# Performance work log

Hardware: AMD Instinct MI355X
Metric: run time of the kernel (lower is better)

The kernel has to match this reference:

```python
import jax, jax.numpy as jnp
import numpy as np

N = 100000
E = 1600000
H = 128
M = 256
L = 6
G = 512          # number of graphs in the batch
A = 95           # num_atom_types
EXTRA = 3        # input_dim - 1
EPS = 1e-5


def swish(x):
    return x * jax.nn.sigmoid(x)


def setup_inputs() -> dict:
    key = jax.random.key(0)
    ks = jax.random.split(key, 16)
    z = jax.random.randint(ks[0], (N, 1), 0, A).astype(jnp.float32)
    extra = jax.random.normal(ks[1], (N, EXTRA), dtype=jnp.float32)
    x = jnp.concatenate([z, extra], axis=1)                     # [N, 4]
    edge_index = jax.random.randint(ks[2], (2, E), 0, N)        # [2, E]
    batch = jnp.sort(jax.random.randint(ks[3], (N,), 0, G))     # [N]
    s = 0.02
    z_embed = jax.random.normal(ks[4], (A, H), dtype=jnp.float32) * s
    extra_w = jax.random.normal(ks[5], (H, EXTRA), dtype=jnp.float32) * (1.0 / np.sqrt(EXTRA))
    extra_b = jnp.zeros((H,), jnp.float32)
    conv_w = jax.random.normal(ks[6], (L, H, H), dtype=jnp.float32) * (1.0 / np.sqrt(H))
    conv_b = jnp.zeros((L, H), jnp.float32)
    gamma = jnp.ones((L, H), jnp.float32)
    beta = jnp.zeros((L, H), jnp.float32)
    mean_scale = jnp.ones((L, H), jnp.float32)
    mlp_w1 = jax.random.normal(ks[7], (L, M, H), dtype=jnp.float32) * (1.0 / np.sqrt(H))
    mlp_b1 = jnp.zeros((L, M), jnp.float32)
    mlp_w2 = jax.random.normal(ks[8], (L, H, M), dtype=jnp.float32) * (1.0 / np.sqrt(M))
    mlp_b2 = jnp.zeros((L, H), jnp.float32)
    return dict(x=x, edge_index=edge_index, batch=batch, z_embed=z_embed,
                extra_w=extra_w, extra_b=extra_b, conv_w=conv_w, conv_b=conv_b,
                gamma=gamma, beta=beta, mean_scale=mean_scale,
                mlp_w1=mlp_w1, mlp_b1=mlp_b1, mlp_w2=mlp_w2, mlp_b2=mlp_b2)


def gnn_forward(x, edge_index, batch, z_embed, extra_w, extra_b, conv_w, conv_b,
                gamma, beta, mean_scale, mlp_w1, mlp_b1, mlp_w2, mlp_b2):
    z = x[:, 0].astype(jnp.int32)
    h = z_embed[z] + x[:, 1:] @ extra_w.T + extra_b                 # [N, H]

    # GCN: add self loops, symmetric normalization (computed once; graph is static)
    loop = jnp.arange(N)
    src = jnp.concatenate([edge_index[0], loop])
    dst = jnp.concatenate([edge_index[1], loop])
    deg = jax.ops.segment_sum(jnp.ones_like(dst, jnp.float32), dst, num_segments=N)
    dinv = jnp.where(deg > 0, jax.lax.rsqrt(jnp.maximum(deg, 1.0)), 0.0)
    norm = (dinv[src] * dinv[dst])[:, None]                         # [E+N, 1]

    cnt = jax.ops.segment_sum(jnp.ones((N,), jnp.float32), batch, num_segments=G)[:, None]
    cnt = jnp.maximum(cnt, 1.0)

    for i in range(L):
        h_res = h
        # GCNConv
        xw = h @ conv_w[i].T
        agg = jax.ops.segment_sum(xw[src] * norm, dst, num_segments=N) + conv_b[i]
        # GraphNorm: gamma * (x - alpha*mean) / sqrt(var + eps) + beta, per graph
        mean = jax.ops.segment_sum(agg, batch, num_segments=G) / cnt   # [G, H]
        sub = agg - mean_scale[i] * mean[batch]
        var = jax.ops.segment_sum(sub * sub, batch, num_segments=G) / cnt
        hn = gamma[i] * sub * jax.lax.rsqrt(var[batch] + EPS) + beta[i]
        ha = swish(hn)
        # residual MLP
        h = swish(swish(ha @ mlp_w1[i].T + mlp_b1[i]) @ mlp_w2[i].T + mlp_b2[i]) + h_res
    return h


def reference(x, edge_index, batch, z_embed, extra_w, extra_b, conv_w, conv_b,
              gamma, beta, mean_scale, mlp_w1, mlp_b1, mlp_w2, mlp_b2):
    return gnn_forward(x, edge_index, batch, z_embed, extra_w, extra_b, conv_w, conv_b,
                       gamma, beta, mean_scale, mlp_w1, mlp_b1, mlp_w2, mlp_b2)
```

## Files before the change

### kernel.cpp

```cpp
#include <hip/hip_runtime.h>

#define NN 100000
#define EE 1600000
#define HH 128
#define MM 256
#define LL 6
#define GG 512
#define SCAN_NB ((NN + 1023) / 1024)

typedef __attribute__((ext_vector_type(8))) short short8;
typedef __attribute__((ext_vector_type(4))) float floatx4;

__device__ __forceinline__ float swishf(float v) {
    return v * __builtin_amdgcn_rcpf(1.0f + __expf(-v));
}

__device__ __forceinline__ unsigned short f2bf(float f) {
    unsigned u = __builtin_bit_cast(unsigned, f);
    unsigned r = u + 0x7FFFu + ((u >> 16) & 1u);
    return (unsigned short)(r >> 16);
}

__device__ __forceinline__ float bf2f(unsigned short u) {
    return __builtin_bit_cast(float, (unsigned)u << 16);
}

__device__ __forceinline__ float2 bf2f2(unsigned u) {
    float2 r;
    r.x = __builtin_bit_cast(float, u << 16);
    r.y = __builtin_bit_cast(float, u & 0xFFFF0000u);
    return r;
}

__device__ __forceinline__ unsigned cvt2bf(float a, float b) {
    unsigned r;
    asm("v_cvt_pk_bf16_f32 %0, %1, %2" : "=v"(r) : "v"(a), "v"(b));
    return r;
}

__device__ __forceinline__ void unpack8(uint4 v, float* a) {
    float2 p0 = bf2f2(v.x), p1 = bf2f2(v.y), p2 = bf2f2(v.z), p3 = bf2f2(v.w);
    a[0] = p0.x; a[1] = p0.y; a[2] = p1.x; a[3] = p1.y;
    a[4] = p2.x; a[5] = p2.y; a[6] = p3.x; a[7] = p3.y;
}

__device__ __forceinline__ uint4 pack8(const float* o) {
    uint4 pk;
    pk.x = cvt2bf(o[0], o[1]);
    pk.y = cvt2bf(o[2], o[3]);
    pk.z = cvt2bf(o[4], o[5]);
    pk.w = cvt2bf(o[6], o[7]);
    return pk;
}

__device__ __forceinline__ uint2 pack4(const float* o) {
    uint2 pk;
    pk.x = cvt2bf(o[0], o[1]);
    pk.y = cvt2bf(o[2], o[3]);
    return pk;
}

__global__ void k_embed(const float* __restrict__ x, const float* __restrict__ z_embed,
                        const float* __restrict__ ew, const float* __restrict__ eb,
                        unsigned short* __restrict__ hb) {
    int idx = blockIdx.x * blockDim.x + threadIdx.x;
    if (idx >= NN * 32) return;
    int n = idx >> 5;
    int c0 = (idx & 31) << 2;
    const float* xr = x + (size_t)n * 4;
    int z = (int)xr[0];
    float x1 = xr[1], x2 = xr[2], x3 = xr[3];
    const float* ze = z_embed + (size_t)z * HH + c0;
    float o[4];
#pragma unroll
    for (int j = 0; j < 4; ++j) {
        int c = c0 + j;
        o[j] = ze[j] + x1 * ew[c * 3 + 0] + x2 * ew[c * 3 + 1] + x3 * ew[c * 3 + 2] + eb[c];
    }
    *(uint2*)(hb + (size_t)n * HH + c0) = pack4(o);
}

__global__ void k_f2bf3(const float* __restrict__ s1, unsigned short* __restrict__ d1, int n1,
                        const float* __restrict__ s2, unsigned short* __restrict__ d2, int n2,
                        const float* __restrict__ s3, unsigned short* __restrict__ d3, int n3) {
    int i = blockIdx.x * blockDim.x + threadIdx.x;
    if (i < n1) {
        d1[i] = f2bf(s1[i]);
    } else if (i < n1 + n2) {
        d2[i - n1] = f2bf(s2[i - n1]);
    } else if (i < n1 + n2 + n3) {
        d3[i - n1 - n2] = f2bf(s3[i - n1 - n2]);
    }
}

__global__ __launch_bounds__(256) void k_degree_p(const int* __restrict__ dst,
                                                  int* __restrict__ deg) {
    int part = blockIdx.x & 7;
    int blk = blockIdx.x >> 3;
    int nb = gridDim.x >> 3;
    int lo = (int)((long long)part * NN / 8);
    int hi = (int)((long long)(part + 1) * NN / 8);
    for (int e = blk * 256 + threadIdx.x; e < EE; e += nb * 256) {
        int d = dst[e];
        if (d >= lo && d < hi) atomicAdd(&deg[d], 1);
    }
}

__global__ void k_dinv(const int* __restrict__ deg, float* __restrict__ dinv) {
    int n = blockIdx.x * blockDim.x + threadIdx.x;
    if (n < NN) dinv[n] = rsqrtf((float)(deg[n] + 1));
}

__global__ void k_scan1(const int* __restrict__ deg, int* __restrict__ bsum) {
    __shared__ int sd[256];
    int t = threadIdx.x;
    int base = blockIdx.x * 1024 + t * 4;
    int s = 0;
#pragma unroll
    for (int j = 0; j < 4; ++j) {
        int i = base + j;
        if (i < NN) s += deg[i];
    }
    sd[t] = s;
    __syncthreads();
    for (int off = 128; off > 0; off >>= 1) {
        if (t < off) sd[t] += sd[t + off];
        __syncthreads();
    }
    if (t == 0) bsum[blockIdx.x] = sd[0];
}

__global__ void k_scan2(const int* __restrict__ bsum, int* __restrict__ boff) {
    __shared__ int sd[128];
    int t = threadIdx.x;
    int v = (t < SCAN_NB) ? bsum[t] : 0;
    sd[t] = v;
    __syncthreads();
    for (int off = 1; off < 128; off <<= 1) {
        int u = (t >= off) ? sd[t - off] : 0;
        __syncthreads();
        sd[t] += u;
        __syncthreads();
    }
    boff[t] = sd[t] - v;
}

__global__ void k_scan3(const int* __restrict__ deg, const int* __restrict__ boff,
                        int* __restrict__ rowptr) {
    __shared__ int sd[256];
    int t = threadIdx.x;
    int base = blockIdx.x * 1024 + t * 4;
    int v[4];
    int s = 0;
#pragma unroll
    for (int j = 0; j < 4; ++j) {
        int i = base + j;
        v[j] = (i < NN) ? deg[i] : 0;
        s += v[j];
    }
    sd[t] = s;
    __syncthreads();
    for (int off = 1; off < 256; off <<= 1) {
        int u = (t >= off) ? sd[t - off] : 0;
        __syncthreads();
        sd[t] += u;
        __syncthreads();
    }
    int run = boff[blockIdx.x] + sd[t] - s;
#pragma unroll
    for (int j = 0; j < 4; ++j) {
        int i = base + j;
        if (i < NN) rowptr[i] = run;
        if (i == NN - 1) rowptr[NN] = run + v[j];
        run += v[j];
    }
}

__global__ __launch_bounds__(256) void k_fill_p(const int* __restrict__ ei,
                                                const int* __restrict__ rowptr,
                                                int* __restrict__ cursor,
                                                int* __restrict__ col) {
    int part = blockIdx.x & 7;
    int blk = blockIdx.x >> 3;
    int nb = gridDim.x >> 3;
    int lo = (int)((long long)part * NN / 8);
    int hi = (int)((long long)(part + 1) * NN / 8);
    for (int e = blk * 256 + threadIdx.x; e < EE; e += nb * 256) {
        int d = ei[EE + e];
        if (d >= lo && d < hi) {
            int p = atomicAdd(&cursor[d], 1);
            col[rowptr[d] + p] = ei[e];
        }
    }
}

__global__ void k_gptr(const int* __restrict__ batch, int* __restrict__ gptr) {
    int n = blockIdx.x * blockDim.x + threadIdx.x;
    if (n >= NN) return;
    int b = batch[n];
    int pb = (n == 0) ? -1 : batch[n - 1];
    for (int g = pb + 1; g <= b; ++g) gptr[g] = n;
    if (n == NN - 1) {
        for (int g = b + 1; g <= GG; ++g) gptr[g] = NN;
    }
}

__global__ __launch_bounds__(256) void k_conv(const unsigned short* __restrict__ A,
                                              const unsigned short* __restrict__ B,
                                              const float* __restrict__ dinv,
                                              unsigned short* __restrict__ Cb) {
    __shared__ unsigned short Bs[128][HH + 8];
    const int tid = threadIdx.x;
    const int wave = tid >> 6;
    const int lane = tid & 63;
    const int quad = lane >> 4;
    const int l16 = lane & 15;
    const int wr = (wave & 1) << 6;
    const int wc = (wave >> 1) << 6;
    const int rowBase = blockIdx.x * 128;

    for (int i = tid; i < 128 * (HH / 8); i += 256) {
        int r = i / (HH / 8);
        int kk = (i % (HH / 8)) * 8;
        int rho = (r & 64) | ((r & 3) << 4) | ((r >> 2) & 15);
        *(uint4*)(&Bs[rho][kk]) = *(const uint4*)(B + (size_t)r * HH + kk);
    }

    floatx4 acc[4][4];
    const floatx4 zed = {0.f, 0.f, 0.f, 0.f};
#pragma unroll
    for (int i = 0; i < 4; ++i)
#pragma unroll
        for (int j = 0; j < 4; ++j) acc[i][j] = zed;

    int ar[4];
#pragma unroll
    for (int i = 0; i < 4; ++i) {
        int r = rowBase + wr + (i << 4) + l16;
        ar[i] = r < NN ? r : NN - 1;
    }

    __syncthreads();

#pragma unroll
    for (int ks = 0; ks < HH / 32; ++ks) {
        int k = (ks << 5) + (quad << 3);
        short8 a[4], b[4];
#pragma unroll
        for (int i = 0; i < 4; ++i) a[i] = *(const short8*)(A + (size_t)ar[i] * HH + k);
#pragma unroll
        for (int j = 0; j < 4; ++j) b[j] = *(const short8*)(&Bs[wc + (j << 4) + l16][k]);
#pragma unroll
        for (int i = 0; i < 4; ++i)
#pragma unroll
            for (int j = 0; j < 4; ++j)
                acc[i][j] =
                    __builtin_amdgcn_mfma_f32_16x16x32_bf16(a[i], b[j], acc[i][j], 0, 0, 0);
    }

    const int c0 = wc + (l16 << 2);
#pragma unroll
    for (int i = 0; i < 4; ++i) {
        int rb = rowBase + wr + (i << 4) + (quad << 2);
#pragma unroll
        for (int reg = 0; reg < 4; ++reg) {
            int r = rb + reg;
            if (r < NN) {
                float dv = dinv[r];
                float o[4];
#pragma unroll
                for (int j = 0; j < 4; ++j) o[j] = acc[i][j][reg] * dv;
                *(uint2*)(Cb + (size_t)r * HH + c0) = pack4(o);
            }
        }
    }
}

__global__ __launch_bounds__(256) void k_agg(const unsigned short* __restrict__ y,
                                             const int* __restrict__ rowptr,
                                             const int* __restrict__ col,
                                             const float* __restrict__ dinv,
                                             const float* __restrict__ cb,
                                             const int* __restrict__ batch,
                                             unsigned short* __restrict__ agg,
                                             float* __restrict__ S1g,
                                             float* __restrict__ S2g) {
    __shared__ float s1s[4][128];
    __shared__ float s2s[4][128];
    __shared__ int sg[4];
    int w = threadIdx.x >> 6;
    int lane = threadIdx.x & 63;
    int grp = lane >> 4;
    int l16 = lane & 15;
    const uint4* yv = (const uint4*)y;
    const int dbase = blockIdx.x * 16 + w * 4;

    float cbv[8];
    {
        float4 c0 = *(const float4*)(cb + l16 * 8);
        float4 c1 = *(const float4*)(cb + l16 * 8 + 4);
        cbv[0] = c0.x; cbv[1] = c0.y; cbv[2] = c0.z; cbv[3] = c0.w;
        cbv[4] = c1.x; cbv[5] = c1.y; cbv[6] = c1.z; cbv[7] = c1.w;
    }

    float sA[8], sB[8];
#pragma unroll
    for (int j = 0; j < 8; ++j) { sA[j] = 0.f; sB[j] = 0.f; }
    int gcur = -1;

    for (int i = 0; i < 4; ++i) {
        int d = dbase + i;
        float acc[8];
#pragma unroll
        for (int j = 0; j < 8; ++j) acc[j] = 0.f;
        if (grp == 0) {
            uint4 v = yv[(size_t)d * 16 + l16];
            unpack8(v, acc);
        }
        int beg = rowptr[d];
        int end = rowptr[d + 1];
        int e = beg + grp;
        for (; e + 4 < end; e += 8) {
            int s0 = col[e];
            int s1 = col[e + 4];
            uint4 v0 = yv[(size_t)s0 * 16 + l16];
            uint4 v1 = yv[(size_t)s1 * 16 + l16];
            float b0[8], b1[8];
            unpack8(v0, b0);
            unpack8(v1, b1);
#pragma unroll
            for (int k = 0; k < 8; ++k) acc[k] += (b0[k] + b1[k]);
        }
        if (e < end) {
            int s0 = col[e];
            uint4 v0 = yv[(size_t)s0 * 16 + l16];
            float b0[8];
            unpack8(v0, b0);
#pragma unroll
            for (int k = 0; k < 8; ++k) acc[k] += b0[k];
        }
#pragma unroll
        for (int j = 0; j < 8; ++j) {
            acc[j] += __shfl_xor(acc[j], 16, 64);
            acc[j] += __shfl_xor(acc[j], 32, 64);
        }
        if (grp == 0) {
            float dv = dinv[d];
            float o[8];
#pragma unroll
            for (int j = 0; j < 8; ++j) o[j] = acc[j] * dv + cbv[j];
            uint4 pk = pack8(o);
            *(uint4*)(agg + (size_t)d * HH + l16 * 8) = pk;
            float2 q0 = bf2f2(pk.x), q1 = bf2f2(pk.y), q2 = bf2f2(pk.z), q3 = bf2f2(pk.w);
            float orv[8] = {q0.x, q0.y, q1.x, q1.y, q2.x, q2.y, q3.x, q3.y};
            int g = batch[d];
            if (g != gcur) {
                if (gcur >= 0) {
#pragma unroll
                    for (int j = 0; j < 8; ++j) {
                        atomicAdd(&S1g[gcur * HH + l16 * 8 + j], sA[j]);
                        atomicAdd(&S2g[gcur * HH + l16 * 8 + j], sB[j]);
                    }
                }
                gcur = g;
#pragma unroll
                for (int j = 0; j < 8; ++j) {
                    sA[j] = orv[j];
                    sB[j] = orv[j] * orv[j];
                }
            } else {
#pragma unroll
                for (int j = 0; j < 8; ++j) {
                    sA[j] += orv[j];
                    sB[j] += orv[j] * orv[j];
                }
            }
        }
    }

    if (grp == 0) {
#pragma unroll
        for (int j = 0; j < 8; ++j) {
            s1s[w][l16 * 8 + j] = sA[j];
            s2s[w][l16 * 8 + j] = sB[j];
        }
        if (l16 == 0) sg[w] = gcur;
    }
    __syncthreads();
    if (threadIdx.x < 128) {
        int c = threadIdx.x;
        int g0 = sg[0], g1 = sg[1], g2 = sg[2], g3 = sg[3];
        if (g0 >= 0 && g0 == g1 && g0 == g2 && g0 == g3) {
            float a = (s1s[0][c] + s1s[1][c]) + (s1s[2][c] + s1s[3][c]);
            float b = (s2s[0][c] + s2s[1][c]) + (s2s[2][c] + s2s[3][c]);
            atomicAdd(&S1g[g0 * HH + c], a);
            atomicAdd(&S2g[g0 * HH + c], b);
        } else {
            int gs[4] = {g0, g1, g2, g3};
#pragma unroll
            for (int ww = 0; ww < 4; ++ww) {
                if (gs[ww] >= 0) {
                    atomicAdd(&S1g[gs[ww] * HH + c], s1s[ww][c]);
                    atomicAdd(&S2g[gs[ww] * HH + c], s2s[ww][c]);
                }
            }
        }
    }
}

__global__ __launch_bounds__(128) void k_finalize(const int* __restrict__ gptr,
                                                  const float* __restrict__ ms,
                                                  const float* __restrict__ gamma,
                                                  const float* __restrict__ beta,
                                                  const float* __restrict__ S1g,
                                                  const float* __restrict__ S2g,
                                                  float* __restrict__ c1,
                                                  float* __restrict__ c0) {
    int g = blockIdx.x;
    int c = threadIdx.x;
    int cnt = gptr[g + 1] - gptr[g];
    float inv = 1.0f / (float)(cnt > 0 ? cnt : 1);
    float S1 = S1g[g * HH + c];
    float S2 = S2g[g * HH + c];
    float m = S1 * inv;
    float msc = ms[c];
    float var = S2 * inv - msc * (2.0f - msc) * m * m;
    float rstd = rsqrtf(var + 1e-5f);
    float c1v = gamma[c] * rstd;
    c1[g * HH + c] = c1v;
    c0[g * HH + c] = beta[c] - c1v * msc * m;
}

__global__ __launch_bounds__(128, 4) void k_mega(const unsigned short* __restrict__ agg,
                                                 const int* __restrict__ batch,
                                                 const float* __restrict__ c1,
                                                 const float* __restrict__ c0,
                                                 const unsigned short* __restrict__ W1,
                                                 const float* __restrict__ b1,
                                                 const unsigned short* __restrict__ W2,
                                                 const float* __restrict__ b2,
                                                 const unsigned short* __restrict__ Wc,
                                                 const float* __restrict__ dinv,
                                                 unsigned short* __restrict__ hb,
                                                 float* __restrict__ h_out,
                                                 unsigned short* __restrict__ y_out,
                                                 int writeF, int doConv) {
    __shared__ unsigned short ha_s[32 * 136];
    __shared__ unsigned short ts[32 * 136];
    const int tid = threadIdx.x;
    const int wave = tid >> 6;
    const int lane = tid & 63;
    const int quad = lane >> 4;
    const int l16 = lane & 15;
    const int rowBase = blockIdx.x * 32;
    const floatx4 zed = {0.f, 0.f, 0.f, 0.f};

    const int wcb = wave << 6;
    const int co = wcb + (l16 << 2);

    {
        int lr = tid >> 2;
        int coff = (tid & 3) << 5;
        int r = rowBase + lr;
        if (r >= NN) r = NN - 1;
        int g = batch[r];
        const float* c1p = c1 + g * HH + coff;
        const float* c0p = c0 + g * HH + coff;
#pragma unroll
        for (int q = 0; q < 4; ++q) {
            uint4 raw = *(const uint4*)(agg + (size_t)r * HH + coff + (q << 3));
            float v[8];
            unpack8(raw, v);
            float4 ca = *(const float4*)(c1p + (q << 3));
            float4 cb4 = *(const float4*)(c1p + (q << 3) + 4);
            float4 da = *(const float4*)(c0p + (q << 3));
            float4 db = *(const float4*)(c0p + (q << 3) + 4);
            float cc1[8] = {ca.x, ca.y, ca.z, ca.w, cb4.x, cb4.y, cb4.z, cb4.w};
            float cc0[8] = {da.x, da.y, da.z, da.w, db.x, db.y, db.z, db.w};
            float o[8];
#pragma unroll
            for (int j = 0; j < 8; ++j) o[j] = swishf(cc1[j] * v[j] + cc0[j]);
            *(uint4*)(&ha_s[lr * 136 + coff + (q << 3)]) = pack8(o);
        }
    }
    __syncthreads();

    {
        floatx4 acc2[2][4];
#pragma unroll
        for (int i = 0; i < 2; ++i)
#pragma unroll
            for (int j = 0; j < 4; ++j) acc2[i][j] = zed;

#pragma unroll
        for (int h = 0; h < 2; ++h) {
            floatx4 acc1[2][4];
#pragma unroll
            for (int i = 0; i < 2; ++i)
#pragma unroll
                for (int j = 0; j < 4; ++j) acc1[i][j] = zed;
#pragma unroll
            for (int ks = 0; ks < 4; ++ks) {
                int k = (ks << 5) + (quad << 3);
                short8 a[2], b[4];
#pragma unroll
                for (int i = 0; i < 2; ++i)
                    a[i] = *(const short8*)(&ha_s[((i << 4) + l16) * 136 + k]);
#pragma unroll
                for (int j = 0; j < 4; ++j)
                    b[j] = *(const short8*)(W1 + (size_t)((h << 7) + co + j) * HH + k);
#pragma unroll
                for (int i = 0; i < 2; ++i)
#pragma unroll
                    for (int j = 0; j < 4; ++j)
                        acc1[i][j] = __builtin_amdgcn_mfma_f32_16x16x32_bf16(a[i], b[j],
                                                                             acc1[i][j], 0, 0, 0);
            }
            float4 b4 = *(const float4*)(b1 + (h << 7) + co);
            float bv1[4] = {b4.x, b4.y, b4.z, b4.w};
#pragma unroll
            for (int i = 0; i < 2; ++i) {
#pragma unroll
                for (int reg = 0; reg < 4; ++reg) {
                    int lr = (i << 4) + (quad << 2) + reg;
                    float o[4];
#pragma unroll
                    for (int j = 0; j < 4; ++j) o[j] = swishf(acc1[i][j][reg] + bv1[j]);
                    *(uint2*)(&ts[lr * 136 + co]) = pack4(o);
                }
            }
            __syncthreads();

#pragma unroll
            for (int ks = 0; ks < 4; ++ks) {
                int k = (ks << 5) + (quad << 3);
                short8 a[2], b[4];
#pragma unroll
                for (int i = 0; i < 2; ++i)
                    a[i] = *(const short8*)(&ts[((i << 4) + l16) * 136 + k]);
#pragma unroll
                for (int j = 0; j < 4; ++j)
                    b[j] = *(const short8*)(W2 + (size_t)(co + j) * MM + (h << 7) + k);
#pragma unroll
                for (int i = 0; i < 2; ++i)
#pragma unroll
                    for (int j = 0; j < 4; ++j)
                        acc2[i][j] = __builtin_amdgcn_mfma_f32_16x16x32_bf16(a[i], b[j],
                                                                             acc2[i][j], 0, 0, 0);
            }
            if (h == 0) __syncthreads();
        }

        float4 b4 = *(const float4*)(b2 + co);
        float bv[4] = {b4.x, b4.y, b4.z, b4.w};
#pragma unroll
        for (int i = 0; i < 2; ++i) {
#pragma unroll
            for (int reg = 0; reg < 4; ++reg) {
                int lr = (i << 4) + (quad << 2) + reg;
                int r = rowBase + lr;
                if (r < NN) {
                    uint2 rv = *(const uint2*)(hb + (size_t)r * HH + co);
                    float2 r01 = bf2f2(rv.x), r23 = bf2f2(rv.y);
                    float o[4];
                    o[0] = swishf(acc2[i][0][reg] + bv[0]) + r01.x;
                    o[1] = swishf(acc2[i][1][reg] + bv[1]) + r01.y;
                    o[2] = swishf(acc2[i][2][reg] + bv[2]) + r23.x;
                    o[3] = swishf(acc2[i][3][reg] + bv[3]) + r23.y;
                    if (doConv) {
                        uint2 pk = pack4(o);
                        *(uint2*)(hb + (size_t)r * HH + co) = pk;
                        *(uint2*)(&ha_s[lr * 136 + co]) = pk;
                    } else {
                        *(float4*)(h_out + (size_t)r * HH + co) =
                            make_float4(o[0], o[1], o[2], o[3]);
                    }
                } else if (doConv) {
                    *(uint2*)(&ha_s[lr * 136 + co]) = make_uint2(0u, 0u);
                }
            }
        }
    }

    if (doConv) {
        __syncthreads();
        floatx4 acc3[2][4];
#pragma unroll
        for (int i = 0; i < 2; ++i)
#pragma unroll
            for (int j = 0; j < 4; ++j) acc3[i][j] = zed;
#pragma unroll
        for (int ks = 0; ks < 4; ++ks) {
            int k = (ks << 5) + (quad << 3);
            short8 a[2], b[4];
#pragma unroll
            for (int i = 0; i < 2; ++i)
                a[i] = *(const short8*)(&ha_s[((i << 4) + l16) * 136 + k]);
#pragma unroll
            for (int j = 0; j < 4; ++j)
                b[j] = *(const short8*)(Wc + (size_t)(co + j) * HH + k);
#pragma unroll
            for (int i = 0; i < 2; ++i)
#pragma unroll
                for (int j = 0; j < 4; ++j)
                    acc3[i][j] =
                        __builtin_amdgcn_mfma_f32_16x16x32_bf16(a[i], b[j], acc3[i][j], 0, 0, 0);
        }
#pragma unroll
        for (int i = 0; i < 2; ++i) {
#pragma unroll
            for (int reg = 0; reg < 4; ++reg) {
                int r = rowBase + (i << 4) + (quad << 2) + reg;
                if (r < NN) {
                    float dv = dinv[r];
                    float o[4];
#pragma unroll
                    for (int j = 0; j < 4; ++j) o[j] = acc3[i][j][reg] * dv;
                    *(uint2*)(y_out + (size_t)r * HH + co) = pack4(o);
                }
            }
        }
    }
}

extern "C" void kernel_launch(void* const* d_in, const int* in_sizes, int n_in,
                              void* d_out, int out_size, void* d_ws, size_t ws_size,
                              hipStream_t stream) {
    const float* x = (const float*)d_in[0];
    const int* ei = (const int*)d_in[1];
    const int* batch = (const int*)d_in[2];
    const float* z_embed = (const float*)d_in[3];
    const float* extra_w = (const float*)d_in[4];
    const float* extra_b = (const float*)d_in[5];
    const float* conv_w = (const float*)d_in[6];
    const float* conv_b = (const float*)d_in[7];
    const float* gamma = (const float*)d_in[8];
    const float* beta = (const float*)d_in[9];
    const float* mean_scale = (const float*)d_in[10];
    const float* mlp_w1 = (const float*)d_in[11];
    const float* mlp_b1 = (const float*)d_in[12];
    const float* mlp_w2 = (const float*)d_in[13];
    const float* mlp_b2 = (const float*)d_in[14];
    float* h_out = (float*)d_out;

    char* wsB = (char*)d_ws;
    size_t off = 0;
    auto alloc = [&](size_t bytes) -> void* {
        void* p = (void*)(wsB + off);
        off = (off + bytes + 255) & ~(size_t)255;
        return p;
    };
    float* dinv = (float*)alloc((size_t)NN * 4);
    int* deg = (int*)alloc((size_t)NN * 4);
    int* cursor = (int*)alloc((size_t)NN * 4);
    int* rowptr = (int*)alloc((size_t)(NN + 1) * 4);
    int* bsum = (int*)alloc(128 * 4);
    int* boff = (int*)alloc(128 * 4);
    int* col = (int*)alloc((size_t)EE * 4);
    int* gptr = (int*)alloc((size_t)(GG + 1) * 4);
    float* c1t = (float*)alloc((size_t)GG * HH * 4);
    float* c0t = (float*)alloc((size_t)GG * HH * 4);
    float* S1g6 = (float*)alloc((size_t)LL * GG * HH * 4);
    float* S2g6 = (float*)alloc((size_t)LL * GG * HH * 4);
    unsigned short* wb =
        (unsigned short*)alloc((size_t)(LL * (HH * HH + MM * HH + HH * MM)) * 2);
    unsigned short* cwb = wb;
    unsigned short* w1b = wb + (size_t)LL * HH * HH;
    unsigned short* w2b = w1b + (size_t)LL * MM * HH;
    unsigned short* hb = (unsigned short*)alloc((size_t)NN * HH * 2);
    unsigned short* ybuf = (unsigned short*)alloc((size_t)NN * HH * 2);
    unsigned short* aggb = (unsigned short*)alloc((size_t)NN * HH * 2);

    hipMemsetAsync(deg, 0, (size_t)NN * 4, stream);
    hipMemsetAsync(cursor, 0, (size_t)NN * 4, stream);
    hipMemsetAsync(S1g6, 0, (size_t)LL * GG * HH * 4, stream);
    hipMemsetAsync(S2g6, 0, (size_t)LL * GG * HH * 4, stream);

    k_embed<<<(NN * 32 + 255) / 256, 256, 0, stream>>>(x, z_embed, extra_w, extra_b, hb);
    {
        int n1 = LL * HH * HH, n2 = LL * MM * HH, n3 = LL * HH * MM;
        int nt = n1 + n2 + n3;
        k_f2bf3<<<(nt + 255) / 256, 256, 0, stream>>>(conv_w, cwb, n1, mlp_w1, w1b, n2,
                                                      mlp_w2, w2b, n3);
    }
    k_degree_p<<<1024, 256, 0, stream>>>(ei + EE, deg);
    k_dinv<<<(NN + 255) / 256, 256, 0, stream>>>(deg, dinv);
    k_scan1<<<SCAN_NB, 256, 0, stream>>>(deg, bsum);
    k_scan2<<<1, 128, 0, stream>>>(bsum, boff);
    k_scan3<<<SCAN_NB, 256, 0, stream>>>(deg, boff, rowptr);
    k_fill_p<<<1024, 256, 0, stream>>>(ei, rowptr, cursor, col);
    k_gptr<<<(NN + 255) / 256, 256, 0, stream>>>(batch, gptr);

    int gconv = (NN + 127) / 128;
    int gmega = (NN + 31) / 32;
    k_conv<<<gconv, 256, 0, stream>>>(hb, cwb, dinv, ybuf);
    for (int i = 0; i < LL; ++i) {
        float* S1 = S1g6 + (size_t)i * GG * HH;
        float* S2 = S2g6 + (size_t)i * GG * HH;
        k_agg<<<NN / 16, 256, 0, stream>>>(ybuf, rowptr, col, dinv,
                                           conv_b + (size_t)i * HH, batch, aggb, S1, S2);
        k_finalize<<<GG, 128, 0, stream>>>(gptr, mean_scale + (size_t)i * HH,
                                           gamma + (size_t)i * HH, beta + (size_t)i * HH,
                                           S1, S2, c1t, c0t);
        k_mega<<<gmega, 128, 0, stream>>>(
            aggb, batch, c1t, c0t, w1b + (size_t)i * MM * HH, mlp_b1 + (size_t)i * MM,
            w2b + (size_t)i * HH * MM, mlp_b2 + (size_t)i * HH,
            cwb + (size_t)(i + 1 < LL ? i + 1 : 0) * HH * HH, dinv, hb, h_out, ybuf,
            i == LL - 1 ? 1 : 0, i < LL - 1 ? 1 : 0);
    }
}
```

Baseline: 1.269 ms.

## Restructure fused MLP kernel to one wave per block and unroll aggregation by four

Result: slower. 1.365 ms (+7.5%).

```diff
diff --git a/kernel.cpp b/kernel.cpp
--- a/kernel.cpp
+++ b/kernel.cpp
@@ -320,18 +320,24 @@
         int beg = rowptr[d];
         int end = rowptr[d + 1];
         int e = beg + grp;
-        for (; e + 4 < end; e += 8) {
+        for (; e + 12 < end; e += 16) {
             int s0 = col[e];
             int s1 = col[e + 4];
+            int s2 = col[e + 8];
+            int s3 = col[e + 12];
             uint4 v0 = yv[(size_t)s0 * 16 + l16];
             uint4 v1 = yv[(size_t)s1 * 16 + l16];
-            float b0[8], b1[8];
+            uint4 v2 = yv[(size_t)s2 * 16 + l16];
+            uint4 v3 = yv[(size_t)s3 * 16 + l16];
+            float b0[8], b1[8], b2[8], b3[8];
             unpack8(v0, b0);
             unpack8(v1, b1);
-#pragma unroll
-            for (int k = 0; k < 8; ++k) acc[k] += (b0[k] + b1[k]);
-        }
-        if (e < end) {
+            unpack8(v2, b2);
+            unpack8(v3, b3);
+#pragma unroll
+            for (int k = 0; k < 8; ++k) acc[k] += (b0[k] + b1[k]) + (b2[k] + b3[k]);
+        }
+        for (; e < end; e += 4) {
             int s0 = col[e];
             uint4 v0 = yv[(size_t)s0 * 16 + l16];
             float b0[8];
@@ -431,43 +437,38 @@
     c0[g * HH + c] = beta[c] - c1v * msc * m;
 }
 
-__global__ __launch_bounds__(128, 4) void k_mega(const unsigned short* __restrict__ agg,
-                                                 const int* __restrict__ batch,
-                                                 const float* __restrict__ c1,
-                                                 const float* __restrict__ c0,
-                                                 const unsigned short* __restrict__ W1,
-                                                 const float* __restrict__ b1,
-                                                 const unsigned short* __restrict__ W2,
-                                                 const float* __restrict__ b2,
-                                                 const unsigned short* __restrict__ Wc,
-                                                 const float* __restrict__ dinv,
-                                                 unsigned short* __restrict__ hb,
-                                                 float* __restrict__ h_out,
-                                                 unsigned short* __restrict__ y_out,
-                                                 int writeF, int doConv) {
+__global__ __launch_bounds__(64, 3) void k_mega(const unsigned short* __restrict__ agg,
+                                                const int* __restrict__ batch,
+                                                const float* __restrict__ c1,
+                                                const float* __restrict__ c0,
+                                                const unsigned short* __restrict__ W1,
+                                                const float* __restrict__ b1,
+                                                const unsigned short* __restrict__ W2,
+                                                const float* __restrict__ b2,
+                                                const unsigned short* __restrict__ Wc,
+                                                const float* __restrict__ dinv,
+                                                unsigned short* __restrict__ hb,
+                                                float* __restrict__ h_out,
+                                                unsigned short* __restrict__ y_out,
+                                                int writeF, int doConv) {
     __shared__ unsigned short ha_s[32 * 136];
-    __shared__ unsigned short ts[32 * 136];
+    __shared__ unsigned short ts[32 * 72];
     const int tid = threadIdx.x;
-    const int wave = tid >> 6;
-    const int lane = tid & 63;
-    const int quad = lane >> 4;
-    const int l16 = lane & 15;
+    const int quad = tid >> 4;
+    const int l16 = tid & 15;
     const int rowBase = blockIdx.x * 32;
+    const int co8 = l16 << 3;
     const floatx4 zed = {0.f, 0.f, 0.f, 0.f};
 
-    const int wcb = wave << 6;
-    const int co = wcb + (l16 << 2);
-
     {
-        int lr = tid >> 2;
-        int coff = (tid & 3) << 5;
+        int lr = tid >> 1;
+        int coff = (tid & 1) << 6;
         int r = rowBase + lr;
-        if (r >= NN) r = NN - 1;
         int g = batch[r];
         const float* c1p = c1 + g * HH + coff;
         const float* c0p = c0 + g * HH + coff;
 #pragma unroll
-        for (int q = 0; q < 4; ++q) {
+        for (int q = 0; q < 8; ++q) {
             uint4 raw = *(const uint4*)(agg + (size_t)r * HH + coff + (q << 3));
             float v[8];
             unpack8(raw, v);
@@ -483,141 +484,135 @@
             *(uint4*)(&ha_s[lr * 136 + coff + (q << 3)]) = pack8(o);
         }
     }
-    __syncthreads();
+
+    floatx4 acc2[2][8];
+#pragma unroll
+    for (int i = 0; i < 2; ++i)
+#pragma unroll
+        for (int j = 0; j < 8; ++j) acc2[i][j] = zed;
+
+#pragma unroll
+    for (int c = 0; c < 4; ++c) {
+        floatx4 acc1[2][4];
+#pragma unroll
+        for (int i = 0; i < 2; ++i)
+#pragma unroll
+            for (int j = 0; j < 4; ++j) acc1[i][j] = zed;
+        const int tco = (c << 6) + (l16 << 2);
+#pragma unroll
+        for (int ks = 0; ks < 4; ++ks) {
+            int k = (ks << 5) + (quad << 3);
+            short8 a[2], b[4];
+#pragma unroll
+            for (int i = 0; i < 2; ++i)
+                a[i] = *(const short8*)(&ha_s[((i << 4) + l16) * 136 + k]);
+#pragma unroll
+            for (int j = 0; j < 4; ++j)
+                b[j] = *(const short8*)(W1 + (size_t)(tco + j) * HH + k);
+#pragma unroll
+            for (int i = 0; i < 2; ++i)
+#pragma unroll
+                for (int j = 0; j < 4; ++j)
+                    acc1[i][j] = __builtin_amdgcn_mfma_f32_16x16x32_bf16(a[i], b[j],
+                                                                         acc1[i][j], 0, 0, 0);
+        }
+        float4 b4 = *(const float4*)(b1 + tco);
+        float bv1[4] = {b4.x, b4.y, b4.z, b4.w};
+#pragma unroll
+        for (int i = 0; i < 2; ++i) {
+#pragma unroll
+            for (int reg = 0; reg < 4; ++reg) {
+                int lr = (i << 4) + (quad << 2) + reg;
+                float o[4];
+#pragma unroll
+                for (int j = 0; j < 4; ++j) o[j] = swishf(acc1[i][j][reg] + bv1[j]);
+                *(uint2*)(&ts[lr * 72 + (l16 << 2)]) = pack4(o);
+            }
+        }
+
+#pragma unroll
+        for (int ks = 0; ks < 2; ++ks) {
+            int k = (ks << 5) + (quad << 3);
+            short8 a[2], b[8];
+#pragma unroll
+            for (int i = 0; i < 2; ++i)
+                a[i] = *(const short8*)(&ts[((i << 4) + l16) * 72 + k]);
+#pragma unroll
+            for (int jo = 0; jo < 8; ++jo)
+                b[jo] = *(const short8*)(W2 + (size_t)(co8 + jo) * MM + (c << 6) + k);
+#pragma unroll
+            for (int i = 0; i < 2; ++i)
+#pragma unroll
+                for (int jo = 0; jo < 8; ++jo)
+                    acc2[i][jo] = __builtin_amdgcn_mfma_f32_16x16x32_bf16(a[i], b[jo],
+                                                                          acc2[i][jo], 0, 0, 0);
+        }
+    }
 
     {
-        floatx4 acc2[2][4];
-#pragma unroll
-        for (int i = 0; i < 2; ++i)
-#pragma unroll
-            for (int j = 0; j < 4; ++j) acc2[i][j] = zed;
-
-#pragma unroll
-        for (int h = 0; h < 2; ++h) {
-            floatx4 acc1[2][4];
-#pragma unroll
-            for (int i = 0; i < 2; ++i)
-#pragma unroll
-                for (int j = 0; j < 4; ++j) acc1[i][j] = zed;
-#pragma unroll
-            for (int ks = 0; ks < 4; ++ks) {
-                int k = (ks << 5) + (quad << 3);
-                short8 a[2], b[4];
-#pragma unroll
-                for (int i = 0; i < 2; ++i)
-                    a[i] = *(const short8*)(&ha_s[((i << 4) + l16) * 136 + k]);
-#pragma unroll
-                for (int j = 0; j < 4; ++j)
-                    b[j] = *(const short8*)(W1 + (size_t)((h << 7) + co + j) * HH + k);
-#pragma unroll
-                for (int i = 0; i < 2; ++i)
-#pragma unroll
-                    for (int j = 0; j < 4; ++j)
-                        acc1[i][j] = __builtin_amdgcn_mfma_f32_16x16x32_bf16(a[i], b[j],
-                                                                             acc1[i][j], 0, 0, 0);
-            }
-            float4 b4 = *(const float4*)(b1 + (h << 7) + co);
-            float bv1[4] = {b4.x, b4.y, b4.z, b4.w};
-#pragma unroll
-            for (int i = 0; i < 2; ++i) {
-#pragma unroll
-                for (int reg = 0; reg < 4; ++reg) {
-                    int lr = (i << 4) + (quad << 2) + reg;
-                    float o[4];
-#pragma unroll
-                    for (int j = 0; j < 4; ++j) o[j] = swishf(acc1[i][j][reg] + bv1[j]);
-                    *(uint2*)(&ts[lr * 136 + co]) = pack4(o);
-                }
-            }
-            __syncthreads();
-
-#pragma unroll
-            for (int ks = 0; ks < 4; ++ks) {
-                int k = (ks << 5) + (quad << 3);
-                short8 a[2], b[4];
-#pragma unroll
-                for (int i = 0; i < 2; ++i)
-                    a[i] = *(const short8*)(&ts[((i << 4) + l16) * 136 + k]);
-#pragma unroll
-                for (int j = 0; j < 4; ++j)
-                    b[j] = *(const short8*)(W2 + (size_t)(co + j) * MM + (h << 7) + k);
-#pragma unroll
-                for (int i = 0; i < 2; ++i)
-#pragma unroll
-                    for (int j = 0; j < 4; ++j)
-                        acc2[i][j] = __builtin_amdgcn_mfma_f32_16x16x32_bf16(a[i], b[j],
-                                                                             acc2[i][j], 0, 0, 0);
-            }
-            if (h == 0) __syncthreads();
-        }
-
-        float4 b4 = *(const float4*)(b2 + co);
-        float bv[4] = {b4.x, b4.y, b4.z, b4.w};
+        float4 e0 = *(const float4*)(b2 + co8);
+        float4 e1 = *(const float4*)(b2 + co8 + 4);
+        float bv[8] = {e0.x, e0.y, e0.z, e0.w, e1.x, e1.y, e1.z, e1.w};
 #pragma unroll
         for (int i = 0; i < 2; ++i) {
 #pragma unroll
             for (int reg = 0; reg < 4; ++reg) {
                 int lr = (i << 4) + (quad << 2) + reg;
                 int r = rowBase + lr;
-                if (r < NN) {
-                    uint2 rv = *(const uint2*)(hb + (size_t)r * HH + co);
-                    float2 r01 = bf2f2(rv.x), r23 = bf2f2(rv.y);
-                    float o[4];
-                    o[0] = swishf(acc2[i][0][reg] + bv[0]) + r01.x;
-                    o[1] = swishf(acc2[i][1][reg] + bv[1]) + r01.y;
-                    o[2] = swishf(acc2[i][2][reg] + bv[2]) + r23.x;
-                    o[3] = swishf(acc2[i][3][reg] + bv[3]) + r23.y;
-                    if (doConv) {
-                        uint2 pk = pack4(o);
-                        *(uint2*)(hb + (size_t)r * HH + co) = pk;
-                        *(uint2*)(&ha_s[lr * 136 + co]) = pk;
-                    } else {
-                        *(float4*)(h_out + (size_t)r * HH + co) =
-                            make_float4(o[0], o[1], o[2], o[3]);
-                    }
-                } else if (doConv) {
-                    *(uint2*)(&ha_s[lr * 136 + co]) = make_uint2(0u, 0u);
+                uint4 rv = *(const uint4*)(hb + (size_t)r * HH + co8);
+                float rr[8];
+                unpack8(rv, rr);
+                float o[8];
+#pragma unroll
+                for (int j = 0; j < 8; ++j)
+                    o[j] = swishf(acc2[i][j][reg] + bv[j]) + rr[j];
+                if (doConv) {
+                    uint4 pk = pack8(o);
+                    *(uint4*)(hb + (size_t)r * HH + co8) = pk;
+                    *(uint4*)(&ha_s[lr * 136 + co8]) = pk;
+                } else {
+                    *(float4*)(h_out + (size_t)r * HH + co8) =
+                        make_float4(o[0], o[1], o[2], o[3]);
+                    *(float4*)(h_out + (size_t)r * HH + co8 + 4) =
+                        make_float4(o[4], o[5], o[6], o[7]);
                 }
             }
         }
     }
 
     if (doConv) {
-        __syncthreads();
-        floatx4 acc3[2][4];
+        floatx4 acc3[2][8];
 #pragma unroll
         for (int i = 0; i < 2; ++i)
 #pragma unroll
-            for (int j = 0; j < 4; ++j) acc3[i][j] = zed;
+            for (int j = 0; j < 8; ++j) acc3[i][j] = zed;
 #pragma unroll
         for (int ks = 0; ks < 4; ++ks) {
             int k = (ks << 5) + (quad << 3);
-            short8 a[2], b[4];
+            short8 a[2], b[8];
 #pragma unroll
             for (int i = 0; i < 2; ++i)
                 a[i] = *(const short8*)(&ha_s[((i << 4) + l16) * 136 + k]);
 #pragma unroll
-            for (int j = 0; j < 4; ++j)
-                b[j] = *(const short8*)(Wc + (size_t)(co + j) * HH + k);
+            for (int jc = 0; jc < 8; ++jc)
+                b[jc] = *(const short8*)(Wc + (size_t)(co8 + jc) * HH + k);
 #pragma unroll
             for (int i = 0; i < 2; ++i)
 #pragma unroll
-                for (int j = 0; j < 4; ++j)
-                    acc3[i][j] =
-                        __builtin_amdgcn_mfma_f32_16x16x32_bf16(a[i], b[j], acc3[i][j], 0, 0, 0);
+                for (int jc = 0; jc < 8; ++jc)
+                    acc3[i][jc] = __builtin_amdgcn_mfma_f32_16x16x32_bf16(a[i], b[jc],
+                                                                          acc3[i][jc], 0, 0, 0);
         }
 #pragma unroll
         for (int i = 0; i < 2; ++i) {
 #pragma unroll
             for (int reg = 0; reg < 4; ++reg) {
                 int r = rowBase + (i << 4) + (quad << 2) + reg;
-                if (r < NN) {
-                    float dv = dinv[r];
-                    float o[4];
-#pragma unroll
-                    for (int j = 0; j < 4; ++j) o[j] = acc3[i][j][reg] * dv;
-                    *(uint2*)(y_out + (size_t)r * HH + co) = pack4(o);
-                }
+                float dv = dinv[r];
+                float o[8];
+#pragma unroll
+                for (int j = 0; j < 8; ++j) o[j] = acc3[i][j][reg] * dv;
+                *(uint4*)(y_out + (size_t)r * HH + co8) = pack8(o);
             }
         }
     }
@@ -692,7 +687,7 @@
     k_gptr<<<(NN + 255) / 256, 256, 0, stream>>>(batch, gptr);
 
     int gconv = (NN + 127) / 128;
-    int gmega = (NN + 31) / 32;
+    int gmega = NN / 32;
     k_conv<<<gconv, 256, 0, stream>>>(hb, cwb, dinv, ybuf);
     for (int i = 0; i < LL; ++i) {
         float* S1 = S1g6 + (size_t)i * GG * HH;
@@ -702,7 +697,7 @@
         k_finalize<<<GG, 128, 0, stream>>>(gptr, mean_scale + (size_t)i * HH,
                                            gamma + (size_t)i * HH, beta + (size_t)i * HH,
                                            S1, S2, c1t, c0t);
-        k_mega<<<gmega, 128, 0, stream>>>(
+        k_mega<<<gmega, 64, 0, stream>>>(
             aggb, batch, c1t, c0t, w1b + (size_t)i * MM * HH, mlp_b1 + (size_t)i * MM,
             w2b + (size_t)i * HH * MM, mlp_b2 + (size_t)i * HH,
             cwb + (size_t)(i + 1 < LL ? i + 1 : 0) * HH * HH, dinv, hb, h_out, ybuf,
```
